# Optimization experiments

Hardware: AMD Instinct MI355X
Metric: run time of the kernel (lower is better)

Reference implementation:

```python
import jax, jax.numpy as jnp
import numpy as np

B, L0, L1, NS, D, H, NL, HM = 16, 512, 256, 32, 256, 8, 4, 4
T = L0 + L1 + NS + 1
HD = D // H
EPS = 1e-5
SCALE = HD ** -0.5


def setup_inputs() -> dict:
    key = jax.random.key(0)
    ks = jax.random.split(key, 20)
    s = 0.02
    return {
        'seq_tokens_0': jax.random.normal(ks[0], (B, L0, D), jnp.float32),
        'seq_tokens_1': jax.random.normal(ks[1], (B, L1, D), jnp.float32),
        'seq_lens_0': jax.random.randint(ks[2], (B,), 0, L0),
        'seq_lens_1': jax.random.randint(ks[3], (B,), 0, L1),
        'ns_tokens': jax.random.normal(ks[4], (B, NS, D), jnp.float32),
        'domain_emb': jax.random.normal(ks[5], (2, D), jnp.float32) * s,
        'cls_token': jax.random.normal(ks[6], (1, 1, D), jnp.float32) * s,
        'ln1_w': jnp.ones((NL, D), jnp.float32),
        'ln1_b': jnp.zeros((NL, D), jnp.float32),
        'qkv_w': jax.random.normal(ks[7], (NL, D, 3 * D), jnp.float32) * s,
        'qkv_b': jnp.zeros((NL, 3 * D), jnp.float32),
        'out_w': jax.random.normal(ks[8], (NL, D, D), jnp.float32) * s,
        'out_b': jnp.zeros((NL, D), jnp.float32),
        'ln2_w': jnp.ones((NL, D), jnp.float32),
        'ln2_b': jnp.zeros((NL, D), jnp.float32),
        'ffn1_w': jax.random.normal(ks[9], (NL, D, HM * D), jnp.float32) * s,
        'ffn1_b': jnp.zeros((NL, HM * D), jnp.float32),
        'ffn2_w': jax.random.normal(ks[10], (NL, HM * D, D), jnp.float32) * s,
        'ffn2_b': jnp.zeros((NL, D), jnp.float32),
        'fln_w': jnp.ones((D,), jnp.float32),
        'fln_b': jnp.zeros((D,), jnp.float32),
    }


def _ln(x, w, b):
    m = jnp.mean(x, -1, keepdims=True)
    v = jnp.var(x, -1, keepdims=True)
    return (x - m) * jax.lax.rsqrt(v + EPS) * w + b


def _build_mask(seq_lens_0, seq_lens_1):
    # static block structure: intra-domain causal, S<->NS bidirectional, CLS sink row
    base = jnp.zeros((T, T), bool)
    base = base.at[:L0, :L0].set(jnp.tril(jnp.ones((L0, L0), bool)))
    base = base.at[L0:L0 + L1, L0:L0 + L1].set(jnp.tril(jnp.ones((L1, L1), bool)))
    ns_s, ns_e = L0 + L1, L0 + L1 + NS
    base = base.at[:ns_s, ns_s:ns_e].set(True)   # S -> NS
    base = base.at[ns_s:ns_e, :ns_e].set(True)   # NS -> S and NS -> NS
    base = base.at[T - 1, :ns_e].set(True)       # CLS reads all S/NS
    base = base.at[T - 1, T - 1].set(True)       # CLS reads itself
    # per-batch padding mask on keys of each seq segment
    kv = jnp.ones((B, T), bool)
    kv = kv.at[:, :L0].set(jnp.arange(L0)[None, :] < seq_lens_0[:, None])
    kv = kv.at[:, L0:L0 + L1].set(jnp.arange(L1)[None, :] < seq_lens_1[:, None])
    return base[None] & kv[:, None, :]  # [B, T, T]


def _attention(x, mask, qkv_w, qkv_b, out_w, out_b):
    qkv = (x @ qkv_w + qkv_b).reshape(B, T, 3, H, HD)
    q, k, v = qkv[:, :, 0], qkv[:, :, 1], qkv[:, :, 2]
    scores = jnp.einsum('bqhd,bkhd->bhqk', q, k) * SCALE
    m = mask[:, None]  # [B,1,T,T]
    s = jnp.where(m, scores, -jnp.inf)
    any_valid = jnp.any(m, -1, keepdims=True)
    mx = jnp.where(any_valid, jnp.max(s, -1, keepdims=True), 0.0)
    e = jnp.exp(s - mx)  # masked entries exp(-inf)=0
    denom = jnp.sum(e, -1, keepdims=True)
    probs = e / jnp.maximum(denom, 1e-30)  # fully-masked rows -> zeros
    out = jnp.einsum('bhqk,bkhd->bqhd', probs, v).reshape(B, T, D)
    return out @ out_w + out_b


def reference(seq_tokens_0, seq_tokens_1, seq_lens_0, seq_lens_1, ns_tokens,
              domain_emb, cls_token, ln1_w, ln1_b, qkv_w, qkv_b, out_w, out_b,
              ln2_w, ln2_b, ffn1_w, ffn1_b, ffn2_w, ffn2_b, fln_w, fln_b):
    t0 = seq_tokens_0 + domain_emb[0][None, None, :]
    t1 = seq_tokens_1 + domain_emb[1][None, None, :]
    cls = jnp.broadcast_to(cls_token, (B, 1, D))
    x = jnp.concatenate([t0, t1, ns_tokens, cls], axis=1)  # [B,T,D]
    mask = _build_mask(seq_lens_0, seq_lens_1)
    for l in range(NL):
        x = x + _attention(_ln(x, ln1_w[l], ln1_b[l]), mask,
                           qkv_w[l], qkv_b[l], out_w[l], out_b[l])
        h = _ln(x, ln2_w[l], ln2_b[l])
        h = jax.nn.gelu(h @ ffn1_w[l] + ffn1_b[l], approximate=False)
        x = x + h @ ffn2_w[l] + ffn2_b[l]
    x = _ln(x, fln_w, fln_b)
    return x[:, -1, :]  # CLS state [B,D]
```

## Files before the change

### kernel.cpp

```cpp
#include <hip/hip_runtime.h>
#include <hip/hip_bf16.h>
#include <math.h>

typedef __attribute__((ext_vector_type(8))) unsigned short ushort8;
typedef __attribute__((ext_vector_type(8))) short short8;
typedef __attribute__((ext_vector_type(4))) float f32x4;
typedef __attribute__((ext_vector_type(4))) unsigned short ushort4v;
typedef __attribute__((ext_vector_type(4))) int i32x4;
typedef unsigned int u32;

namespace {
constexpr int B = 16, L0 = 512, L1 = 256, NS = 32, D = 256, H = 8, NL = 4, HM = 4;
constexpr int T = L0 + L1 + NS + 1;
constexpr int HD = D / H;
constexpr int NS_S = L0 + L1;
constexpr int TPAD = 832;
constexpr int ROWP = 13312;
constexpr float EPS = 1e-5f;
constexpr float SCL2  = 0.17677669529663687f * 1.4426950408889634f;
}

__device__ __forceinline__ ushort f2bf(float f) {
    union { float f; unsigned u; } v; v.f = f;
    return (ushort)((v.u + 0x7fffu + ((v.u >> 16) & 1u)) >> 16);
}

__device__ __forceinline__ u32 cvtpk(float a, float b) {
    u32 r;
    asm("v_cvt_pk_bf16_f32 %0, %1, %2" : "=v"(r) : "v"(a), "v"(b));
    return r;
}

__device__ __forceinline__ void gload_lds16(const void* g, void* l) {
    __builtin_amdgcn_global_load_lds(
        (const __attribute__((address_space(1))) u32*)g,
        (__attribute__((address_space(3))) u32*)l, 16, 0, 0);
}

__device__ __forceinline__ int offs_of(const int* __restrict__ l0,
                                       const int* __restrict__ l1, int b) {
    int acc = 0;
    for (int j = 0; j < b; ++j) acc += ((l0[j] + l1[j] + 96) >> 6) << 6;
    return acc;
}

__global__ __launch_bounds__(256) void k_wprep_all(
    const float* __restrict__ qkvw, const float* __restrict__ outw,
    const float* __restrict__ f1w, const float* __restrict__ f2w,
    ushort* __restrict__ qkvt, ushort* __restrict__ outt,
    ushort* __restrict__ f1t, ushort* __restrict__ f2t)
{
    int id = blockIdx.x;
    const float* src; ushort* dst; int K, N;
    if (id < 768)        { src = qkvw; dst = qkvt; K = 256;  N = 768;  }
    else if (id < 1024)  { id -= 768;  src = outw; dst = outt; K = 256; N = 256; }
    else if (id < 2048)  { id -= 1024; src = f1w;  dst = f1t;  K = 256; N = 1024; }
    else                 { id -= 2048; src = f2w;  dst = f2t;  K = 1024; N = 256; }
    const int ktiles = K >> 5, per = ktiles * (N >> 5);
    const int layer = id / per, rem = id % per;
    const int kb = (rem % ktiles) * 32, nb = (rem / ktiles) * 32;
    src += (size_t)layer * K * N; dst += (size_t)layer * K * N;

    __shared__ float t[32][33];
    const int c = threadIdx.x & 31, r8 = threadIdx.x >> 5;
#pragma unroll
    for (int rr = 0; rr < 32; rr += 8)
        t[r8 + rr][c] = src[(size_t)(kb + r8 + rr) * N + nb + c];
    __syncthreads();
#pragma unroll
    for (int rr = 0; rr < 32; rr += 8)
        dst[(size_t)(nb + r8 + rr) * K + kb + c] = f2bf(t[c][r8 + rr]);
}

__global__ __launch_bounds__(256) void k_build_ln(
    const float* __restrict__ s0, const float* __restrict__ s1,
    const float* __restrict__ ns, const float* __restrict__ dom,
    const float* __restrict__ cls, const float* __restrict__ lnw,
    const float* __restrict__ lnb, const int* __restrict__ len0,
    const int* __restrict__ len1, float* __restrict__ x, ushort* __restrict__ xn)
{
    const int wid = threadIdx.x >> 6, lane = threadIdx.x & 63;
    const int row = blockIdx.x * 4 + wid;
    if (row >= ROWP) return;
    const int d0 = lane * 4;

    int bsel = -1, t = -1, acc = 0;
    for (int j = 0; j < 16; ++j) {
        const int n0 = len0[j], n1 = len1[j];
        const int nvj = n0 + n1 + 33;
        const int cap = ((nvj + 63) >> 6) << 6;
        if (row < acc + cap) {
            const int loc = row - acc;
            if (loc < nvj)
                t = (loc < n0) ? loc
                  : (loc < n0 + n1) ? (L0 + loc - n0)
                  : (NS_S + loc - n0 - n1);
            bsel = j;
            break;
        }
        acc += cap;
    }
    if (bsel < 0 || t < 0) {
        float4 z = {0.f, 0.f, 0.f, 0.f};
        *(float4*)(x + (size_t)row * D + d0) = z;
        ushort4v z4 = {0, 0, 0, 0};
        *(ushort4v*)(xn + (size_t)row * D + d0) = z4;
        return;
    }
    const int b = bsel;
    float4 v;
    if (t < L0) {
        v = *(const float4*)(s0 + ((size_t)b * L0 + t) * D + d0);
        float4 dm = *(const float4*)(dom + d0);
        v.x += dm.x; v.y += dm.y; v.z += dm.z; v.w += dm.w;
    } else if (t < NS_S) {
        v = *(const float4*)(s1 + ((size_t)b * L1 + (t - L0)) * D + d0);
        float4 dm = *(const float4*)(dom + D + d0);
        v.x += dm.x; v.y += dm.y; v.z += dm.z; v.w += dm.w;
    } else if (t < NS_S + NS) {
        v = *(const float4*)(ns + ((size_t)b * NS + (t - NS_S)) * D + d0);
    } else {
        v = *(const float4*)(cls + d0);
    }
    *(float4*)(x + (size_t)row * D + d0) = v;
    float s  = v.x + v.y + v.z + v.w;
    float ss = v.x * v.x + v.y * v.y + v.z * v.z + v.w * v.w;
#pragma unroll
    for (int o = 32; o; o >>= 1) { s += __shfl_xor(s, o); ss += __shfl_xor(ss, o); }
    const float mean = s * (1.f / D);
    const float var  = ss * (1.f / D) - mean * mean;
    const float r = rsqrtf(var + EPS);
    float4 wv = *(const float4*)(lnw + d0);
    float4 bv = *(const float4*)(lnb + d0);
    ushort4v o4;
    o4[0] = f2bf((v.x - mean) * r * wv.x + bv.x);
    o4[1] = f2bf((v.y - mean) * r * wv.y + bv.y);
    o4[2] = f2bf((v.z - mean) * r * wv.z + bv.z);
    o4[3] = f2bf((v.w - mean) * r * wv.w + bv.w);
    *(ushort4v*)(xn + (size_t)row * D + d0) = o4;
}

template<bool GELU, bool OBF, bool CLSW>
__global__ __launch_bounds__(256) void k_gemm_mfma(
    const ushort* __restrict__ A, const ushort* __restrict__ Wt,
    const float* __restrict__ bias, void* __restrict__ Cout,
    const int* __restrict__ len0, const int* __restrict__ len1,
    int N, int K, int nOff)
{
    __shared__ ushort As[2][128 * 64];
    __shared__ ushort Bs[2][128 * 64];
    const int tid = threadIdx.x;
    const int lane = tid & 63, w = tid >> 6;
    const int lo = lane & 15, g = lane >> 4;
    const int wr = w >> 1, wc = w & 1;
    int m0;
    if (CLSW) {
        const int bb = blockIdx.x;
        const int clsrow = offs_of(len0, len1, bb) + len0[bb] + len1[bb] + 32;
        m0 = (clsrow >> 7) << 7;
    } else {
        m0 = blockIdx.x * 128;
        if (m0 >= offs_of(len0, len1, 16)) return;
    }
    const int n0 = (blockIdx.y + nOff) * 128;

    f32x4 zero = {0.f, 0.f, 0.f, 0.f};
    f32x4 acc[4][4];
#pragma unroll
    for (int mi = 0; mi < 4; ++mi)
#pragma unroll
        for (int ni = 0; ni < 4; ++ni) acc[mi][ni] = zero;

    const ushort* srcA[4];
    const ushort* srcB[4];
    int ldsOff[4];
#pragma unroll
    for (int i = 0; i < 4; ++i) {
        const int idx16 = (w * 4 + i) * 64 + lane;
        const int row = idx16 >> 3;
        const int scb = ((idx16 & 7) * 16) ^ ((row & 7) << 4);
        srcA[i] = A  + (size_t)(m0 + row) * K + (scb >> 1);
        srcB[i] = Wt + (size_t)(n0 + row) * K + (scb >> 1);
        ldsOff[i] = (w * 4 + i) * 512;
    }

    const int NT = K >> 6;
#pragma unroll
    for (int i = 0; i < 4; ++i) {
        gload_lds16(srcA[i], &As[0][ldsOff[i]]);
        gload_lds16(srcB[i], &Bs[0][ldsOff[i]]);
    }
    asm volatile("s_waitcnt vmcnt(0)");
    __syncthreads();

    for (int t = 0; t < NT; ++t) {
        const int buf = t & 1;
        if (t + 1 < NT) {
            const int nb = buf ^ 1, ko = (t + 1) * 64;
#pragma unroll
            for (int i = 0; i < 4; ++i) {
                gload_lds16(srcA[i] + ko, &As[nb][ldsOff[i]]);
                gload_lds16(srcB[i] + ko, &Bs[nb][ldsOff[i]]);
            }
        }
#pragma unroll
        for (int kk = 0; kk < 2; ++kk) {
            const int kb = (kk * 64 + g * 16) ^ ((lo & 7) << 4);
            short8 af[4], bfr[4];
#pragma unroll
            for (int mi = 0; mi < 4; ++mi)
                af[mi] = *(const short8*)&As[buf][(wr * 64 + mi * 16 + lo) * 64 + (kb >> 1)];
#pragma unroll
            for (int ni = 0; ni < 4; ++ni)
                bfr[ni] = *(const short8*)&Bs[buf][(wc * 64 + ni * 16 + lo) * 64 + (kb >> 1)];
#pragma unroll
            for (int mi = 0; mi < 4; ++mi)
#pragma unroll
                for (int ni = 0; ni < 4; ++ni)
                    acc[mi][ni] = __builtin_amdgcn_mfma_f32_16x16x32_bf16(
                        af[mi], bfr[ni], acc[mi][ni], 0, 0, 0);
        }
        asm volatile("s_waitcnt vmcnt(0)");
        __syncthreads();
    }

    float bv[4];
#pragma unroll
    for (int ni = 0; ni < 4; ++ni) bv[ni] = bias[n0 + wc * 64 + ni * 16 + lo];
#pragma unroll
    for (int mi = 0; mi < 4; ++mi) {
#pragma unroll
        for (int i = 0; i < 4; ++i) {
            const int row = m0 + wr * 64 + mi * 16 + g * 4 + i;
#pragma unroll
            for (int ni = 0; ni < 4; ++ni) {
                const int col = n0 + wc * 64 + ni * 16 + lo;
                float v = acc[mi][ni][i] + bv[ni];
                if (GELU) v = 0.5f * v * (1.0f + erff(v * 0.70710678118654752f));
                if (OBF) ((ushort*)Cout)[(size_t)row * N + col] = f2bf(v);
                else     ((float*)Cout)[(size_t)row * N + col] = v;
            }
        }
    }
}

template<int MODE, bool CLSW>
__global__ __launch_bounds__(256) void k_gemm_fused(
    const ushort* __restrict__ A, const ushort* __restrict__ Wt,
    const float* __restrict__ bias, const float* __restrict__ res,
    const float* __restrict__ lnw, const float* __restrict__ lnb,
    float* __restrict__ xout, ushort* __restrict__ xnout,
    float* __restrict__ dout, const int* __restrict__ len0,
    const int* __restrict__ len1, int K)
{
    __shared__ ushort As[2][64 * 64];
    __shared__ ushort Bs[2][256 * 64];
    __shared__ float redS[64][4];
    __shared__ float redQ[64][4];
    const int tid = threadIdx.x;
    const int lane = tid & 63, w = tid >> 6;
    const int lo = lane & 15, g = lane >> 4;
    int m0, clsrow = -1, bb = 0;
    if (CLSW) {
        bb = blockIdx.x;
        clsrow = offs_of(len0, len1, bb) + len0[bb] + len1[bb] + 32;
        m0 = (clsrow >> 6) << 6;
    } else {
        m0 = blockIdx.x * 64;
        if (m0 >= offs_of(len0, len1, 16)) return;
    }

    f32x4 zero = {0.f, 0.f, 0.f, 0.f};
    f32x4 acc[4][4];
#pragma unroll
    for (int mi = 0; mi < 4; ++mi)
#pragma unroll
        for (int ni = 0; ni < 4; ++ni) acc[mi][ni] = zero;

    const ushort* srcA[2]; int ldsOffA[2];
    const ushort* srcB[8]; int ldsOffB[8];
#pragma unroll
    for (int j = 0; j < 2; ++j) {
        const int idx16 = j * 256 + tid;
        const int row = idx16 >> 3;
        const int scb = ((idx16 & 7) * 16) ^ ((row & 7) << 4);
        srcA[j] = A + (size_t)(m0 + row) * K + (scb >> 1);
        ldsOffA[j] = idx16 * 8;
    }
#pragma unroll
    for (int j = 0; j < 8; ++j) {
        const int idx16 = j * 256 + tid;
        const int row = idx16 >> 3;
        const int scb = ((idx16 & 7) * 16) ^ ((row & 7) << 4);
        srcB[j] = Wt + (size_t)row * K + (scb >> 1);
        ldsOffB[j] = idx16 * 8;
    }

    const int NT = K >> 6;
#pragma unroll
    for (int j = 0; j < 2; ++j) gload_lds16(srcA[j], &As[0][ldsOffA[j]]);
#pragma unroll
    for (int j = 0; j < 8; ++j) gload_lds16(srcB[j], &Bs[0][ldsOffB[j]]);
    asm volatile("s_waitcnt vmcnt(0)");
    __syncthreads();

    for (int t = 0; t < NT; ++t) {
        const int buf = t & 1;
        if (t + 1 < NT) {
            const int nb = buf ^ 1, ko = (t + 1) * 64;
#pragma unroll
            for (int j = 0; j < 2; ++j) gload_lds16(srcA[j] + ko, &As[nb][ldsOffA[j]]);
#pragma unroll
            for (int j = 0; j < 8; ++j) gload_lds16(srcB[j] + ko, &Bs[nb][ldsOffB[j]]);
        }
#pragma unroll
        for (int kk = 0; kk < 2; ++kk) {
            const int kb = (kk * 64 + g * 16) ^ ((lo & 7) << 4);
            short8 af[4], bfr[4];
#pragma unroll
            for (int mi = 0; mi < 4; ++mi)
                af[mi] = *(const short8*)&As[buf][(mi * 16 + lo) * 64 + (kb >> 1)];
#pragma unroll
            for (int ni = 0; ni < 4; ++ni)
                bfr[ni] = *(const short8*)&Bs[buf][(w * 64 + ni * 16 + lo) * 64 + (kb >> 1)];
#pragma unroll
            for (int mi = 0; mi < 4; ++mi)
#pragma unroll
                for (int ni = 0; ni < 4; ++ni)
                    acc[mi][ni] = __builtin_amdgcn_mfma_f32_16x16x32_bf16(
                        af[mi], bfr[ni], acc[mi][ni], 0, 0, 0);
        }
        asm volatile("s_waitcnt vmcnt(0)");
        __syncthreads();
    }

    float bv[4], lw[4], lb[4];
#pragma unroll
    for (int ni = 0; ni < 4; ++ni) {
        const int c = w * 64 + ni * 16 + lo;
        bv[ni] = bias[c]; lw[ni] = lnw[c]; lb[ni] = lnb[c];
    }
#pragma unroll
    for (int mi = 0; mi < 4; ++mi) {
#pragma unroll
        for (int i = 0; i < 4; ++i) {
            const int r64 = mi * 16 + g * 4 + i;
            const int row = m0 + r64;
            float s = 0.f, q = 0.f;
#pragma unroll
            for (int ni = 0; ni < 4; ++ni) {
                const int col = w * 64 + ni * 16 + lo;
                float v = acc[mi][ni][i] + bv[ni] + res[(size_t)row * 256 + col];
                acc[mi][ni][i] = v;
                s += v; q += v * v;
            }
            s += __shfl_xor(s, 1); q += __shfl_xor(q, 1);
            s += __shfl_xor(s, 2); q += __shfl_xor(q, 2);
            s += __shfl_xor(s, 4); q += __shfl_xor(q, 4);
            s += __shfl_xor(s, 8); q += __shfl_xor(q, 8);
            if (lo == 0) { redS[r64][w] = s; redQ[r64][w] = q; }
        }
    }
    __syncthreads();
#pragma unroll
    for (int mi = 0; mi < 4; ++mi) {
#pragma unroll
        for (int i = 0; i < 4; ++i) {
            const int r64 = mi * 16 + g * 4 + i;
            const int row = m0 + r64;
            const float S = redS[r64][0] + redS[r64][1] + redS[r64][2] + redS[r64][3];
            const float Q = redQ[r64][0] + redQ[r64][1] + redQ[r64][2] + redQ[r64][3];
            const float mean = S * (1.f / 256.f);
            const float var  = Q * (1.f / 256.f) - mean * mean;
            const float rstd = rsqrtf(var + EPS);
            if (MODE == 0) {
#pragma unroll
                for (int ni = 0; ni < 4; ++ni) {
                    const int col = w * 64 + ni * 16 + lo;
                    const float v = acc[mi][ni][i];
                    xout[(size_t)row * 256 + col] = v;
                    xnout[(size_t)row * 256 + col] = f2bf((v - mean) * rstd * lw[ni] + lb[ni]);
                }
            } else {
                if (row == clsrow) {
#pragma unroll
                    for (int ni = 0; ni < 4; ++ni) {
                        const int col = w * 64 + ni * 16 + lo;
                        dout[(size_t)bb * 256 + col] =
                            (acc[mi][ni][i] - mean) * rstd * lw[ni] + lb[ni];
                    }
                }
            }
        }
    }
}

__global__ __launch_bounds__(256) void k_repack(
    const ushort* __restrict__ qkv, ushort* __restrict__ Kb, ushort* __restrict__ Vt,
    const int* __restrict__ len0, const int* __restrict__ len1)
{
    const int bh = blockIdx.x, tt = blockIdx.y;
    const int b = bh >> 3, h = bh & 7;
    const int nv = len0[b] + len1[b] + 33;
    const int t0 = tt * 64;
    if (t0 >= nv) return;
    const int base = offs_of(len0, len1, b);
    const int tid = threadIdx.x;
    const int r = tid >> 2, c = tid & 3;
    __shared__ ushort vtile[64][40];
    const ushort* kp = qkv + (size_t)(base + t0 + r) * 768 + 256 + h * HD + c * 8;
    ushort8 k8 = *(const ushort8*)kp;
    ushort8 v8 = *(const ushort8*)(kp + 256);
    *(ushort8*)(Kb + ((size_t)bh * TPAD + t0 + r) * HD + c * 8) = k8;
    *(ushort8*)&vtile[r][c * 8] = v8;
    __syncthreads();
    const int d = tid >> 3, cc = tid & 7;
    ushort8 o;
#pragma unroll
    for (int j = 0; j < 8; ++j) o[j] = vtile[cc * 8 + j][d];
    *(ushort8*)(Vt + ((size_t)bh * HD + d) * TPAD + t0 + cc * 8) = o;
}

template<bool CLSONLY>
__global__ __launch_bounds__(64) void k_flash(
    const ushort* __restrict__ qkv, const ushort* __restrict__ Kb,
    const ushort* __restrict__ Vt, const int* __restrict__ len0,
    const int* __restrict__ len1, ushort* __restrict__ out)
{
    const int bh = blockIdx.x;
    const int b = bh >> 3, h = bh & 7;
    const int clen0 = len0[b], cns = clen0 + len1[b];
    const int nv = cns + 33;
    const int tl = (nv - 1) >> 6, tn0 = cns >> 6;
    int qt;
    if (CLSONLY) qt = tl;
    else { qt = 12 - (int)blockIdx.y; if (qt > tl) return; }

    const int base = offs_of(len0, len1, b);
    const int w = blockIdx.z;
    const int lane = threadIdx.x;
    const int lo = lane & 15, g = lane >> 4;
    const int b4 = g & 1, b5 = g >> 1;
    const int q0t = qt * 64;
    const int qmin = q0t + w * 16, qmax = qmin + 15;
    const int q = qmin + lo;

    short8 qf = *(const short8*)(qkv + (size_t)(base + q) * 768 + h * HD + g * 8);

    const ushort* Kbase = Kb + (size_t)bh * TPAD * HD;
    const ushort* Vbase = Vt + (size_t)bh * HD * TPAD;

    f32x4 acc0 = {0.f, 0.f, 0.f, 0.f}, acc1 = {0.f, 0.f, 0.f, 0.f};
    float mrow = -1e30f, srow = 0.f;

    const int kts = (qmin >= clen0 && qmax < cns) ? (clen0 >> 6) : 0;
    const int nc = qt - kts + 1;
    const int estart = (qt + 1 > tn0) ? (qt + 1) : tn0;
    const int extra = (tl >= estart) ? (tl - estart + 1) : 0;
    const int ntiles = nc + extra;
    auto ktile = [&](int it) { return (it < nc) ? (kts + it) : (estart + (it - nc)); };

    auto xpose = [&](const u32 C0[4], const u32 C1[4], short8& pb0, short8& pb1) {
        u32 pb0u[4], pb1u[4];
#pragma unroll
        for (int n = 0; n < 4; ++n) {
            const u32 F0 = (u32)__shfl_xor((int)C0[n], 16);
            const u32 F1 = (u32)__shfl_xor((int)C1[n], 16);
            const u32 G00 = b4 ? F0 : C0[n];
            const u32 G01 = b4 ? C0[n] : F0;
            const u32 G10 = b4 ? F1 : C1[n];
            const u32 G11 = b4 ? C1[n] : F1;
            const u32 H00 = (u32)__shfl_xor((int)G00, 32);
            const u32 H01 = (u32)__shfl_xor((int)G01, 32);
            const u32 H10 = (u32)__shfl_xor((int)G10, 32);
            const u32 H11 = (u32)__shfl_xor((int)G11, 32);
            const bool keep = (b5 == b4);
            const u32 S00 = keep ? G00 : H00;
            const u32 S01 = keep ? G01 : H01;
            const u32 S10 = keep ? G10 : H10;
            const u32 S11 = keep ? G11 : H11;
            const bool take = (b5 == (n & 1));
            if ((n >> 1) == 0) {
                pb0u[0] = take ? S00 : pb0u[0];
                pb0u[1] = take ? S10 : pb0u[1];
                pb0u[2] = take ? S01 : pb0u[2];
                pb0u[3] = take ? S11 : pb0u[3];
            } else {
                pb1u[0] = take ? S00 : pb1u[0];
                pb1u[1] = take ? S10 : pb1u[1];
                pb1u[2] = take ? S01 : pb1u[2];
                pb1u[3] = take ? S11 : pb1u[3];
            }
        }
        i32x4 t0 = { (int)pb0u[0], (int)pb0u[1], (int)pb0u[2], (int)pb0u[3] };
        i32x4 t1 = { (int)pb1u[0], (int)pb1u[1], (int)pb1u[2], (int)pb1u[3] };
        pb0 = __builtin_bit_cast(short8, t0);
        pb1 = __builtin_bit_cast(short8, t1);
    };

    short8 kf[4];
    {
        const int k0 = ktile(0) * 64;
#pragma unroll
        for (int n = 0; n < 4; ++n)
            kf[n] = *(const short8*)(Kbase + (size_t)(k0 + n * 16 + lo) * HD + g * 8);
    }

    for (int it = 0; it < ntiles; ++it) {
        const int k0 = ktile(it) * 64;

        const bool interior =
            (qmax < clen0 && k0 + 63 <= qmin) ||
            (qmin >= clen0 && qmax < cns && k0 >= clen0 && k0 + 63 <= qmin) ||
            (qmin >= cns && k0 + 63 < cns + 32);

        const ushort* V0 = Vbase + k0;
        short8 a00 = *(const short8*)(V0 + (size_t)lo * TPAD + g * 8);
        short8 a01 = *(const short8*)(V0 + (size_t)lo * TPAD + 32 + g * 8);
        short8 a10 = *(const short8*)(V0 + (size_t)(16 + lo) * TPAD + g * 8);
        short8 a11 = *(const short8*)(V0 + (size_t)(16 + lo) * TPAD + 32 + g * 8);

        float pv[4][4];
        float tmax = -1e30f;
#pragma unroll
        for (int n = 0; n < 4; ++n) {
            f32x4 z = {0.f, 0.f, 0.f, 0.f};
            f32x4 sn = __builtin_amdgcn_mfma_f32_16x16x32_bf16(kf[n], qf, z, 0, 0, 0);
            if (interior) {
#pragma unroll
                for (int i = 0; i < 4; ++i) {
                    pv[n][i] = sn[i] * SCL2;
                    tmax = fmaxf(tmax, pv[n][i]);
                }
            } else {
#pragma unroll
                for (int i = 0; i < 4; ++i) {
                    const int k = k0 + n * 16 + g * 4 + i;
                    const bool win = (k >= cns) & (k < cns + 32);
                    bool m;
                    if (q < clen0)         m = (k <= q) | win;
                    else if (q < cns)      m = ((k >= clen0) & (k <= q)) | win;
                    else if (q < cns + 32) m = (k < cns + 32);
                    else                   m = (k < cns + 32) | (k == q);
                    const float sv = m ? sn[i] * SCL2 : -1e30f;
                    pv[n][i] = sv;
                    tmax = fmaxf(tmax, sv);
                }
            }
        }

        short8 kf2[4];
        if (it + 1 < ntiles) {
            const int k1 = ktile(it + 1) * 64;
#pragma unroll
            for (int n = 0; n < 4; ++n)
                kf2[n] = *(const short8*)(Kbase + (size_t)(k1 + n * 16 + lo) * HD + g * 8);
        }

        tmax = fmaxf(tmax, __shfl_xor(tmax, 16));
        tmax = fmaxf(tmax, __shfl_xor(tmax, 32));
        const float mnew = fmaxf(mrow, tmax);
        if (mnew > mrow) {
            const float scl = exp2f(mrow - mnew);
            srow *= scl;
#pragma unroll
            for (int i = 0; i < 4; ++i) { acc0[i] *= scl; acc1[i] *= scl; }
            mrow = mnew;
        }

        u32 C0[4], C1[4];
        float psum = 0.f;
#pragma unroll
        for (int n = 0; n < 4; ++n) {
            float e0 = (pv[n][0] > -1e29f) ? exp2f(pv[n][0] - mrow) : 0.f;
            float e1 = (pv[n][1] > -1e29f) ? exp2f(pv[n][1] - mrow) : 0.f;
            float e2 = (pv[n][2] > -1e29f) ? exp2f(pv[n][2] - mrow) : 0.f;
            float e3 = (pv[n][3] > -1e29f) ? exp2f(pv[n][3] - mrow) : 0.f;
            psum += (e0 + e1) + (e2 + e3);
            C0[n] = cvtpk(e0, e1);
            C1[n] = cvtpk(e2, e3);
        }
        psum += __shfl_xor(psum, 16);
        psum += __shfl_xor(psum, 32);
        srow += psum;

        short8 pb0, pb1;
        xpose(C0, C1, pb0, pb1);
        acc0 = __builtin_amdgcn_mfma_f32_16x16x32_bf16(a00, pb0, acc0, 0, 0, 0);
        acc0 = __builtin_amdgcn_mfma_f32_16x16x32_bf16(a01, pb1, acc0, 0, 0, 0);
        acc1 = __builtin_amdgcn_mfma_f32_16x16x32_bf16(a10, pb0, acc1, 0, 0, 0);
        acc1 = __builtin_amdgcn_mfma_f32_16x16x32_bf16(a11, pb1, acc1, 0, 0, 0);

#pragma unroll
        for (int n = 0; n < 4; ++n) kf[n] = kf2[n];
    }

    if (q < nv) {
        const float inv = 1.f / fmaxf(srow, 1e-30f);
        ushort* orow = out + (size_t)(base + q) * D + h * HD;
        *(u32*)(orow + g * 4)          = cvtpk(acc0[0] * inv, acc0[1] * inv);
        *(u32*)(orow + g * 4 + 2)      = cvtpk(acc0[2] * inv, acc0[3] * inv);
        *(u32*)(orow + 16 + g * 4)     = cvtpk(acc1[0] * inv, acc1[1] * inv);
        *(u32*)(orow + 16 + g * 4 + 2) = cvtpk(acc1[2] * inv, acc1[3] * inv);
    }
}

extern "C" void kernel_launch(void* const* d_in, const int* in_sizes, int n_in,
                              void* d_out, int out_size, void* d_ws, size_t ws_size,
                              hipStream_t stream)
{
    const float* seq0 = (const float*)d_in[0];
    const float* seq1 = (const float*)d_in[1];
    const int*   len0 = (const int*)d_in[2];
    const int*   len1 = (const int*)d_in[3];
    const float* nst  = (const float*)d_in[4];
    const float* dom  = (const float*)d_in[5];
    const float* cls  = (const float*)d_in[6];
    const float* ln1w = (const float*)d_in[7];
    const float* ln1b = (const float*)d_in[8];
    const float* qkvw = (const float*)d_in[9];
    const float* qkvb = (const float*)d_in[10];
    const float* outw = (const float*)d_in[11];
    const float* outb = (const float*)d_in[12];
    const float* ln2w = (const float*)d_in[13];
    const float* ln2b = (const float*)d_in[14];
    const float* f1w  = (const float*)d_in[15];
    const float* f1b  = (const float*)d_in[16];
    const float* f2w  = (const float*)d_in[17];
    const float* f2b  = (const float*)d_in[18];
    const float* flnw = (const float*)d_in[19];
    const float* flnb = (const float*)d_in[20];

    float*  x   = (float*)d_ws;
    ushort* xn  = (ushort*)(x + (size_t)ROWP * D);
    ushort* big = xn + (size_t)ROWP * D;
    ushort* Kb  = big + (size_t)ROWP * HM * D;
    ushort* Vt  = Kb + (size_t)B * H * TPAD * HD;
    ushort* qkvw_t = Vt + (size_t)B * H * TPAD * HD;
    ushort* outw_t = qkvw_t + (size_t)NL * 768 * 256;
    ushort* f1w_t  = outw_t + (size_t)NL * 256 * 256;
    ushort* f2w_t  = f1w_t  + (size_t)NL * 1024 * 256;

    k_wprep_all<<<3072, 256, 0, stream>>>(qkvw, outw, f1w, f2w,
                                          qkvw_t, outw_t, f1w_t, f2w_t);
    k_build_ln<<<ROWP / 4, 256, 0, stream>>>(seq0, seq1, nst, dom, cls,
                                             ln1w, ln1b, len0, len1, x, xn);

    const int gmm = ROWP / 128;
    const int gf  = ROWP / 64;

    for (int l = 0; l < NL; ++l) {
        const bool last = (l == NL - 1);
        if (!last) {
            k_gemm_mfma<false, true, false><<<dim3(gmm, 6), 256, 0, stream>>>(
                xn, qkvw_t + (size_t)l * 768 * 256, qkvb + (size_t)l * 3 * D, big,
                len0, len1, 3 * D, D, 0);
        } else {
            k_gemm_mfma<false, true, false><<<dim3(gmm, 4), 256, 0, stream>>>(
                xn, qkvw_t + (size_t)l * 768 * 256, qkvb + (size_t)l * 3 * D, big,
                len0, len1, 3 * D, D, 2);
            k_gemm_mfma<false, true, true><<<dim3(B, 2), 256, 0, stream>>>(
                xn, qkvw_t + (size_t)l * 768 * 256, qkvb + (size_t)l * 3 * D, big,
                len0, len1, 3 * D, D, 0);
        }
        k_repack<<<dim3(B * H, 13), 256, 0, stream>>>(big, Kb, Vt, len0, len1);
        if (!last)
            k_flash<false><<<dim3(B * H, 13, 4), 64, 0, stream>>>(
                big, Kb, Vt, len0, len1, xn);
        else
            k_flash<true><<<dim3(B * H, 1, 4), 64, 0, stream>>>(
                big, Kb, Vt, len0, len1, xn);
        if (!last)
            k_gemm_fused<0, false><<<gf, 256, 0, stream>>>(
                xn, outw_t + (size_t)l * 256 * 256, outb + (size_t)l * D, x,
                ln2w + l * D, ln2b + l * D, x, xn, nullptr, len0, len1, D);
        else
            k_gemm_fused<0, true><<<B, 256, 0, stream>>>(
                xn, outw_t + (size_t)l * 256 * 256, outb + (size_t)l * D, x,
                ln2w + l * D, ln2b + l * D, x, xn, nullptr, len0, len1, D);
        if (!last)
            k_gemm_mfma<true, true, false><<<dim3(gmm, 8), 256, 0, stream>>>(
                xn, f1w_t + (size_t)l * 1024 * 256, f1b + (size_t)l * HM * D, big,
                len0, len1, HM * D, D, 0);
        else
            k_gemm_mfma<true, true, true><<<dim3(B, 8), 256, 0, stream>>>(
                xn, f1w_t + (size_t)l * 1024 * 256, f1b + (size_t)l * HM * D, big,
                len0, len1, HM * D, D, 0);
        if (!last)
            k_gemm_fused<0, false><<<gf, 256, 0, stream>>>(
                big, f2w_t + (size_t)l * 256 * 1024, f2b + (size_t)l * D, x,
                ln1w + (l + 1) * D, ln1b + (l + 1) * D, x, xn, nullptr,
                len0, len1, HM * D);
        else
            k_gemm_fused<1, true><<<B, 256, 0, stream>>>(
                big, f2w_t + (size_t)l * 256 * 1024, f2b + (size_t)l * D, x,
                flnw, flnb, nullptr, nullptr, (float*)d_out, len0, len1, HM * D);
    }
}
```

Measured before the change: 458.4 us.

## Fuse out-projection, LN2, FFN1 with GELU and FFN2 into one per-tile kernel

Replaces the separate out-proj+LN, FFN1+GELU and FFN2+LN kernels with one kernel per 64-row tile. The tile keeps the normalised activations and the FFN hidden chunks in swizzled LDS, so the 1024-wide hidden tensor never goes to global memory and two launches per layer disappear. In exchange, weight fragments are read directly from global memory without LDS staging or double buffering. The 64KB LDS footprint and large register use may also lower occupancy.

```diff
diff --git a/kernel.cpp b/kernel.cpp
--- a/kernel.cpp
+++ b/kernel.cpp
@@ -140,7 +140,7 @@
     *(ushort4v*)(xn + (size_t)row * D + d0) = o4;
 }
 
-template<bool GELU, bool OBF, bool CLSW>
+template<bool OBF, bool CLSW>
 __global__ __launch_bounds__(256) void k_gemm_mfma(
     const ushort* __restrict__ A, const ushort* __restrict__ Wt,
     const float* __restrict__ bias, void* __restrict__ Cout,
@@ -236,160 +236,8 @@
             for (int ni = 0; ni < 4; ++ni) {
                 const int col = n0 + wc * 64 + ni * 16 + lo;
                 float v = acc[mi][ni][i] + bv[ni];
-                if (GELU) v = 0.5f * v * (1.0f + erff(v * 0.70710678118654752f));
                 if (OBF) ((ushort*)Cout)[(size_t)row * N + col] = f2bf(v);
                 else     ((float*)Cout)[(size_t)row * N + col] = v;
-            }
-        }
-    }
-}
-
-template<int MODE, bool CLSW>
-__global__ __launch_bounds__(256) void k_gemm_fused(
-    const ushort* __restrict__ A, const ushort* __restrict__ Wt,
-    const float* __restrict__ bias, const float* __restrict__ res,
-    const float* __restrict__ lnw, const float* __restrict__ lnb,
-    float* __restrict__ xout, ushort* __restrict__ xnout,
-    float* __restrict__ dout, const int* __restrict__ len0,
-    const int* __restrict__ len1, int K)
-{
-    __shared__ ushort As[2][64 * 64];
-    __shared__ ushort Bs[2][256 * 64];
-    __shared__ float redS[64][4];
-    __shared__ float redQ[64][4];
-    const int tid = threadIdx.x;
-    const int lane = tid & 63, w = tid >> 6;
-    const int lo = lane & 15, g = lane >> 4;
-    int m0, clsrow = -1, bb = 0;
-    if (CLSW) {
-        bb = blockIdx.x;
-        clsrow = offs_of(len0, len1, bb) + len0[bb] + len1[bb] + 32;
-        m0 = (clsrow >> 6) << 6;
-    } else {
-        m0 = blockIdx.x * 64;
-        if (m0 >= offs_of(len0, len1, 16)) return;
-    }
-
-    f32x4 zero = {0.f, 0.f, 0.f, 0.f};
-    f32x4 acc[4][4];
-#pragma unroll
-    for (int mi = 0; mi < 4; ++mi)
-#pragma unroll
-        for (int ni = 0; ni < 4; ++ni) acc[mi][ni] = zero;
-
-    const ushort* srcA[2]; int ldsOffA[2];
-    const ushort* srcB[8]; int ldsOffB[8];
-#pragma unroll
-    for (int j = 0; j < 2; ++j) {
-        const int idx16 = j * 256 + tid;
-        const int row = idx16 >> 3;
-        const int scb = ((idx16 & 7) * 16) ^ ((row & 7) << 4);
-        srcA[j] = A + (size_t)(m0 + row) * K + (scb >> 1);
-        ldsOffA[j] = idx16 * 8;
-    }
-#pragma unroll
-    for (int j = 0; j < 8; ++j) {
-        const int idx16 = j * 256 + tid;
-        const int row = idx16 >> 3;
-        const int scb = ((idx16 & 7) * 16) ^ ((row & 7) << 4);
-        srcB[j] = Wt + (size_t)row * K + (scb >> 1);
-        ldsOffB[j] = idx16 * 8;
-    }
-
-    const int NT = K >> 6;
-#pragma unroll
-    for (int j = 0; j < 2; ++j) gload_lds16(srcA[j], &As[0][ldsOffA[j]]);
-#pragma unroll
-    for (int j = 0; j < 8; ++j) gload_lds16(srcB[j], &Bs[0][ldsOffB[j]]);
-    asm volatile("s_waitcnt vmcnt(0)");
-    __syncthreads();
-
-    for (int t = 0; t < NT; ++t) {
-        const int buf = t & 1;
-        if (t + 1 < NT) {
-            const int nb = buf ^ 1, ko = (t + 1) * 64;
-#pragma unroll
-            for (int j = 0; j < 2; ++j) gload_lds16(srcA[j] + ko, &As[nb][ldsOffA[j]]);
-#pragma unroll
-            for (int j = 0; j < 8; ++j) gload_lds16(srcB[j] + ko, &Bs[nb][ldsOffB[j]]);
-        }
-#pragma unroll
-        for (int kk = 0; kk < 2; ++kk) {
-            const int kb = (kk * 64 + g * 16) ^ ((lo & 7) << 4);
-            short8 af[4], bfr[4];
-#pragma unroll
-            for (int mi = 0; mi < 4; ++mi)
-                af[mi] = *(const short8*)&As[buf][(mi * 16 + lo) * 64 + (kb >> 1)];
-#pragma unroll
-            for (int ni = 0; ni < 4; ++ni)
-                bfr[ni] = *(const short8*)&Bs[buf][(w * 64 + ni * 16 + lo) * 64 + (kb >> 1)];
-#pragma unroll
-            for (int mi = 0; mi < 4; ++mi)
-#pragma unroll
-                for (int ni = 0; ni < 4; ++ni)
-                    acc[mi][ni] = __builtin_amdgcn_mfma_f32_16x16x32_bf16(
-                        af[mi], bfr[ni], acc[mi][ni], 0, 0, 0);
-        }
-        asm volatile("s_waitcnt vmcnt(0)");
-        __syncthreads();
-    }
-
-    float bv[4], lw[4], lb[4];
-#pragma unroll
-    for (int ni = 0; ni < 4; ++ni) {
-        const int c = w * 64 + ni * 16 + lo;
-        bv[ni] = bias[c]; lw[ni] = lnw[c]; lb[ni] = lnb[c];
-    }
-#pragma unroll
-    for (int mi = 0; mi < 4; ++mi) {
-#pragma unroll
-        for (int i = 0; i < 4; ++i) {
-            const int r64 = mi * 16 + g * 4 + i;
-            const int row = m0 + r64;
-            float s = 0.f, q = 0.f;
-#pragma unroll
-            for (int ni = 0; ni < 4; ++ni) {
-                const int col = w * 64 + ni * 16 + lo;
-                float v = acc[mi][ni][i] + bv[ni] + res[(size_t)row * 256 + col];
-                acc[mi][ni][i] = v;
-                s += v; q += v * v;
-            }
-            s += __shfl_xor(s, 1); q += __shfl_xor(q, 1);
-            s += __shfl_xor(s, 2); q += __shfl_xor(q, 2);
-            s += __shfl_xor(s, 4); q += __shfl_xor(q, 4);
-            s += __shfl_xor(s, 8); q += __shfl_xor(q, 8);
-            if (lo == 0) { redS[r64][w] = s; redQ[r64][w] = q; }
-        }
-    }
-    __syncthreads();
-#pragma unroll
-    for (int mi = 0; mi < 4; ++mi) {
-#pragma unroll
-        for (int i = 0; i < 4; ++i) {
-            const int r64 = mi * 16 + g * 4 + i;
-            const int row = m0 + r64;
-            const float S = redS[r64][0] + redS[r64][1] + redS[r64][2] + redS[r64][3];
-            const float Q = redQ[r64][0] + redQ[r64][1] + redQ[r64][2] + redQ[r64][3];
-            const float mean = S * (1.f / 256.f);
-            const float var  = Q * (1.f / 256.f) - mean * mean;
-            const float rstd = rsqrtf(var + EPS);
-            if (MODE == 0) {
-#pragma unroll
-                for (int ni = 0; ni < 4; ++ni) {
-                    const int col = w * 64 + ni * 16 + lo;
-                    const float v = acc[mi][ni][i];
-                    xout[(size_t)row * 256 + col] = v;
-                    xnout[(size_t)row * 256 + col] = f2bf((v - mean) * rstd * lw[ni] + lb[ni]);
-                }
-            } else {
-                if (row == clsrow) {
-#pragma unroll
-                    for (int ni = 0; ni < 4; ++ni) {
-                        const int col = w * 64 + ni * 16 + lo;
-                        dout[(size_t)bb * 256 + col] =
-                            (acc[mi][ni][i] - mean) * rstd * lw[ni] + lb[ni];
-                    }
-                }
             }
         }
     }
@@ -605,6 +453,243 @@
     }
 }
 
+template<int MODE, bool CLSW>
+__global__ __launch_bounds__(256) void k_layer2h(
+    const ushort* __restrict__ ao, const ushort* __restrict__ Wot,
+    const float* __restrict__ bo, const ushort* __restrict__ W1t,
+    const float* __restrict__ b1, const ushort* __restrict__ W2t,
+    const float* __restrict__ b2, const float* __restrict__ ln2w,
+    const float* __restrict__ ln2b, const float* __restrict__ lnnw,
+    const float* __restrict__ lnnb, float* __restrict__ x,
+    ushort* __restrict__ xn, float* __restrict__ dout,
+    const int* __restrict__ len0, const int* __restrict__ len1)
+{
+    __shared__ ushort xs[64 * 256];
+    __shared__ ushort hs[64 * 256];
+    float* redS = (float*)hs;
+    float* redQ = redS + 256;
+    const int tid = threadIdx.x, lane = tid & 63, w = tid >> 6;
+    const int lo = lane & 15, g = lane >> 4;
+    int m0, clsrow = -1, bb = 0;
+    if (CLSW) {
+        bb = blockIdx.x;
+        clsrow = offs_of(len0, len1, bb) + len0[bb] + len1[bb] + 32;
+        m0 = (clsrow >> 6) << 6;
+    } else {
+        m0 = blockIdx.x * 64;
+        if (m0 >= offs_of(len0, len1, 16)) return;
+    }
+
+    f32x4 zero = {0.f, 0.f, 0.f, 0.f};
+
+    f32x4 acc[4][4];
+#pragma unroll
+    for (int mi = 0; mi < 4; ++mi)
+#pragma unroll
+        for (int ni = 0; ni < 4; ++ni) acc[mi][ni] = zero;
+#pragma unroll
+    for (int kk = 0; kk < 8; ++kk) {
+        const int kb = kk * 32 + g * 8;
+        short8 af[4], bf[4];
+#pragma unroll
+        for (int mi = 0; mi < 4; ++mi)
+            af[mi] = *(const short8*)(ao + (size_t)(m0 + mi * 16 + lo) * 256 + kb);
+#pragma unroll
+        for (int ni = 0; ni < 4; ++ni)
+            bf[ni] = *(const short8*)(Wot + (size_t)(w * 64 + ni * 16 + lo) * 256 + kb);
+#pragma unroll
+        for (int mi = 0; mi < 4; ++mi)
+#pragma unroll
+            for (int ni = 0; ni < 4; ++ni)
+                acc[mi][ni] = __builtin_amdgcn_mfma_f32_16x16x32_bf16(
+                    af[mi], bf[ni], acc[mi][ni], 0, 0, 0);
+    }
+    float bv[4], l2w_[4], l2b_[4];
+#pragma unroll
+    for (int ni = 0; ni < 4; ++ni) {
+        const int c = w * 64 + ni * 16 + lo;
+        bv[ni] = bo[c]; l2w_[ni] = ln2w[c]; l2b_[ni] = ln2b[c];
+    }
+#pragma unroll
+    for (int mi = 0; mi < 4; ++mi) {
+#pragma unroll
+        for (int i = 0; i < 4; ++i) {
+            const int r64 = mi * 16 + g * 4 + i;
+            const int row = m0 + r64;
+            float s = 0.f, q = 0.f;
+#pragma unroll
+            for (int ni = 0; ni < 4; ++ni) {
+                const int col = w * 64 + ni * 16 + lo;
+                float v = acc[mi][ni][i] + bv[ni] + x[(size_t)row * 256 + col];
+                acc[mi][ni][i] = v;
+                s += v; q += v * v;
+            }
+            s += __shfl_xor(s, 1); q += __shfl_xor(q, 1);
+            s += __shfl_xor(s, 2); q += __shfl_xor(q, 2);
+            s += __shfl_xor(s, 4); q += __shfl_xor(q, 4);
+            s += __shfl_xor(s, 8); q += __shfl_xor(q, 8);
+            if (lo == 0) { redS[r64 * 4 + w] = s; redQ[r64 * 4 + w] = q; }
+        }
+    }
+    __syncthreads();
+#pragma unroll
+    for (int mi = 0; mi < 4; ++mi) {
+#pragma unroll
+        for (int i = 0; i < 4; ++i) {
+            const int r64 = mi * 16 + g * 4 + i;
+            const int row = m0 + r64;
+            const float S = redS[r64 * 4 + 0] + redS[r64 * 4 + 1] + redS[r64 * 4 + 2] + redS[r64 * 4 + 3];
+            const float Q = redQ[r64 * 4 + 0] + redQ[r64 * 4 + 1] + redQ[r64 * 4 + 2] + redQ[r64 * 4 + 3];
+            const float mean = S * (1.f / 256.f);
+            const float var  = Q * (1.f / 256.f) - mean * mean;
+            const float rstd = rsqrtf(var + EPS);
+#pragma unroll
+            for (int ni = 0; ni < 4; ++ni) {
+                const int col = w * 64 + ni * 16 + lo;
+                const float v = acc[mi][ni][i];
+                x[(size_t)row * 256 + col] = v;
+                const u32 a = (u32)(((r64 * 256 + col) * 2) ^ ((r64 & 7) << 4));
+                *(ushort*)((char*)xs + a) = f2bf((v - mean) * rstd * l2w_[ni] + l2b_[ni]);
+            }
+        }
+    }
+    __syncthreads();
+
+    f32x4 o2[4][4];
+#pragma unroll
+    for (int mi = 0; mi < 4; ++mi)
+#pragma unroll
+        for (int ni = 0; ni < 4; ++ni) o2[mi][ni] = zero;
+
+    for (int c = 0; c < 4; ++c) {
+        f32x4 hc[4][4];
+#pragma unroll
+        for (int mi = 0; mi < 4; ++mi)
+#pragma unroll
+            for (int ni = 0; ni < 4; ++ni) hc[mi][ni] = zero;
+#pragma unroll
+        for (int kk = 0; kk < 8; ++kk) {
+            const int kb = kk * 32 + g * 8;
+            short8 af[4], bf[4];
+#pragma unroll
+            for (int mi = 0; mi < 4; ++mi) {
+                const int r = mi * 16 + lo;
+                const u32 a = (u32)(((r * 256 + kb) * 2) ^ ((lo & 7) << 4));
+                af[mi] = *(const short8*)((const char*)xs + a);
+            }
+#pragma unroll
+            for (int ni = 0; ni < 4; ++ni)
+                bf[ni] = *(const short8*)(W1t + (size_t)(c * 256 + w * 64 + ni * 16 + lo) * 256 + kb);
+#pragma unroll
+            for (int mi = 0; mi < 4; ++mi)
+#pragma unroll
+                for (int ni = 0; ni < 4; ++ni)
+                    hc[mi][ni] = __builtin_amdgcn_mfma_f32_16x16x32_bf16(
+                        af[mi], bf[ni], hc[mi][ni], 0, 0, 0);
+        }
+        float b1v[4];
+#pragma unroll
+        for (int ni = 0; ni < 4; ++ni) b1v[ni] = b1[c * 256 + w * 64 + ni * 16 + lo];
+#pragma unroll
+        for (int mi = 0; mi < 4; ++mi) {
+#pragma unroll
+            for (int i = 0; i < 4; ++i) {
+                const int r64 = mi * 16 + g * 4 + i;
+#pragma unroll
+                for (int ni = 0; ni < 4; ++ni) {
+                    const int col = w * 64 + ni * 16 + lo;
+                    float v = hc[mi][ni][i] + b1v[ni];
+                    v = 0.5f * v * (1.0f + erff(v * 0.70710678118654752f));
+                    const u32 a = (u32)(((r64 * 256 + col) * 2) ^ ((r64 & 7) << 4));
+                    *(ushort*)((char*)hs + a) = f2bf(v);
+                }
+            }
+        }
+        __syncthreads();
+#pragma unroll
+        for (int kk = 0; kk < 8; ++kk) {
+            const int kb = kk * 32 + g * 8;
+            short8 af[4], bf[4];
+#pragma unroll
+            for (int mi = 0; mi < 4; ++mi) {
+                const int r = mi * 16 + lo;
+                const u32 a = (u32)(((r * 256 + kb) * 2) ^ ((lo & 7) << 4));
+                af[mi] = *(const short8*)((const char*)hs + a);
+            }
+#pragma unroll
+            for (int ni = 0; ni < 4; ++ni)
+                bf[ni] = *(const short8*)(W2t + (size_t)(w * 64 + ni * 16 + lo) * 1024 + c * 256 + kb);
+#pragma unroll
+            for (int mi = 0; mi < 4; ++mi)
+#pragma unroll
+                for (int ni = 0; ni < 4; ++ni)
+                    o2[mi][ni] = __builtin_amdgcn_mfma_f32_16x16x32_bf16(
+                        af[mi], bf[ni], o2[mi][ni], 0, 0, 0);
+        }
+        __syncthreads();
+    }
+
+    float b2v[4], lnw_[4], lnb_[4];
+#pragma unroll
+    for (int ni = 0; ni < 4; ++ni) {
+        const int c = w * 64 + ni * 16 + lo;
+        b2v[ni] = b2[c]; lnw_[ni] = lnnw[c]; lnb_[ni] = lnnb[c];
+    }
+#pragma unroll
+    for (int mi = 0; mi < 4; ++mi) {
+#pragma unroll
+        for (int i = 0; i < 4; ++i) {
+            const int r64 = mi * 16 + g * 4 + i;
+            const int row = m0 + r64;
+            float s = 0.f, q = 0.f;
+#pragma unroll
+            for (int ni = 0; ni < 4; ++ni) {
+                const int col = w * 64 + ni * 16 + lo;
+                float v = o2[mi][ni][i] + b2v[ni] + x[(size_t)row * 256 + col];
+                o2[mi][ni][i] = v;
+                s += v; q += v * v;
+            }
+            s += __shfl_xor(s, 1); q += __shfl_xor(q, 1);
+            s += __shfl_xor(s, 2); q += __shfl_xor(q, 2);
+            s += __shfl_xor(s, 4); q += __shfl_xor(q, 4);
+            s += __shfl_xor(s, 8); q += __shfl_xor(q, 8);
+            if (lo == 0) { redS[r64 * 4 + w] = s; redQ[r64 * 4 + w] = q; }
+        }
+    }
+    __syncthreads();
+#pragma unroll
+    for (int mi = 0; mi < 4; ++mi) {
+#pragma unroll
+        for (int i = 0; i < 4; ++i) {
+            const int r64 = mi * 16 + g * 4 + i;
+            const int row = m0 + r64;
+            const float S = redS[r64 * 4 + 0] + redS[r64 * 4 + 1] + redS[r64 * 4 + 2] + redS[r64 * 4 + 3];
+            const float Q = redQ[r64 * 4 + 0] + redQ[r64 * 4 + 1] + redQ[r64 * 4 + 2] + redQ[r64 * 4 + 3];
+            const float mean = S * (1.f / 256.f);
+            const float var  = Q * (1.f / 256.f) - mean * mean;
+            const float rstd = rsqrtf(var + EPS);
+            if (MODE == 0) {
+#pragma unroll
+                for (int ni = 0; ni < 4; ++ni) {
+                    const int col = w * 64 + ni * 16 + lo;
+                    const float v = o2[mi][ni][i];
+                    x[(size_t)row * 256 + col] = v;
+                    xn[(size_t)row * 256 + col] = f2bf((v - mean) * rstd * lnw_[ni] + lnb_[ni]);
+                }
+            } else {
+                if (row == clsrow) {
+#pragma unroll
+                    for (int ni = 0; ni < 4; ++ni) {
+                        const int col = w * 64 + ni * 16 + lo;
+                        dout[(size_t)bb * 256 + col] =
+                            (o2[mi][ni][i] - mean) * rstd * lnw_[ni] + lnb_[ni];
+                    }
+                }
+            }
+        }
+    }
+}
+
 extern "C" void kernel_launch(void* const* d_in, const int* in_sizes, int n_in,
                               void* d_out, int out_size, void* d_ws, size_t ws_size,
                               hipStream_t stream)
@@ -652,14 +737,14 @@
     for (int l = 0; l < NL; ++l) {
         const bool last = (l == NL - 1);
         if (!last) {
-            k_gemm_mfma<false, true, false><<<dim3(gmm, 6), 256, 0, stream>>>(
+            k_gemm_mfma<true, false><<<dim3(gmm, 6), 256, 0, stream>>>(
                 xn, qkvw_t + (size_t)l * 768 * 256, qkvb + (size_t)l * 3 * D, big,
                 len0, len1, 3 * D, D, 0);
         } else {
-            k_gemm_mfma<false, true, false><<<dim3(gmm, 4), 256, 0, stream>>>(
+            k_gemm_mfma<true, false><<<dim3(gmm, 4), 256, 0, stream>>>(
                 xn, qkvw_t + (size_t)l * 768 * 256, qkvb + (size_t)l * 3 * D, big,
                 len0, len1, 3 * D, D, 2);
-            k_gemm_mfma<false, true, true><<<dim3(B, 2), 256, 0, stream>>>(
+            k_gemm_mfma<true, true><<<dim3(B, 2), 256, 0, stream>>>(
                 xn, qkvw_t + (size_t)l * 768 * 256, qkvb + (size_t)l * 3 * D, big,
                 len0, len1, 3 * D, D, 0);
         }
@@ -671,29 +756,19 @@
             k_flash<true><<<dim3(B * H, 1, 4), 64, 0, stream>>>(
                 big, Kb, Vt, len0, len1, xn);
         if (!last)
-            k_gemm_fused<0, false><<<gf, 256, 0, stream>>>(
-                xn, outw_t + (size_t)l * 256 * 256, outb + (size_t)l * D, x,
-                ln2w + l * D, ln2b + l * D, x, xn, nullptr, len0, len1, D);
+            k_layer2h<0, false><<<gf, 256, 0, stream>>>(
+                xn, outw_t + (size_t)l * 256 * 256, outb + (size_t)l * D,
+                f1w_t + (size_t)l * 1024 * 256, f1b + (size_t)l * HM * D,
+                f2w_t + (size_t)l * 256 * 1024, f2b + (size_t)l * D,
+                ln2w + l * D, ln2b + l * D,
+                ln1w + (l + 1) * D, ln1b + (l + 1) * D,
+                x, xn, nullptr, len0, len1);
         else
-            k_gemm_fused<0, true><<<B, 256, 0, stream>>>(
-                xn, outw_t + (size_t)l * 256 * 256, outb + (size_t)l * D, x,
-                ln2w + l * D, ln2b + l * D, x, xn, nullptr, len0, len1, D);
-        if (!last)
-            k_gemm_mfma<true, true, false><<<dim3(gmm, 8), 256, 0, stream>>>(
-                xn, f1w_t + (size_t)l * 1024 * 256, f1b + (size_t)l * HM * D, big,
-                len0, len1, HM * D, D, 0);
-        else
-            k_gemm_mfma<true, true, true><<<dim3(B, 8), 256, 0, stream>>>(
-                xn, f1w_t + (size_t)l * 1024 * 256, f1b + (size_t)l * HM * D, big,
-                len0, len1, HM * D, D, 0);
-        if (!last)
-            k_gemm_fused<0, false><<<gf, 256, 0, stream>>>(
-                big, f2w_t + (size_t)l * 256 * 1024, f2b + (size_t)l * D, x,
-                ln1w + (l + 1) * D, ln1b + (l + 1) * D, x, xn, nullptr,
-                len0, len1, HM * D);
-        else
-            k_gemm_fused<1, true><<<B, 256, 0, stream>>>(
-                big, f2w_t + (size_t)l * 256 * 1024, f2b + (size_t)l * D, x,
-                flnw, flnb, nullptr, nullptr, (float*)d_out, len0, len1, HM * D);
-    }
-}
+            k_layer2h<1, true><<<B, 256, 0, stream>>>(
+                xn, outw_t + (size_t)l * 256 * 256, outb + (size_t)l * D,
+                f1w_t + (size_t)l * 1024 * 256, f1b + (size_t)l * HM * D,
+                f2w_t + (size_t)l * 256 * 1024, f2b + (size_t)l * D,
+                ln2w + l * D, ln2b + l * D, flnw, flnb,
+                x, xn, (float*)d_out, len0, len1);
+    }
+}
```

After: 523.3 us. 14.2% more time.
